# Kernel tuning notes

Hardware: AMD Instinct MI355X
Metric: run time of the kernel (lower is better)

The kernel has to match this reference:

```python
import jax, jax.numpy as jnp
import numpy as np

N = 100_000          # nodes
E = 1_600_000        # edges
NUM_LABELS = 1000
LBL_DIM = 64
BBOX_DIM = 64        # bbox MLP output dim
HID = 128            # gnn hidden = out channels; gnn in = LBL_DIM + BBOX_DIM = 128


def setup_inputs() -> dict:
    key = jax.random.key(0)
    ks = jax.random.split(key, 14)
    label = jax.random.randint(ks[0], (N,), 0, NUM_LABELS)
    bbox = jax.random.uniform(ks[1], (N, 4), dtype=jnp.float32)
    edge_index = jax.random.randint(ks[2], (2, E), 0, N)
    emb_table = jax.random.normal(ks[3], (NUM_LABELS, LBL_DIM), dtype=jnp.float32) * 0.02
    mlp_w1 = jax.random.normal(ks[4], (4, BBOX_DIM), dtype=jnp.float32) * 0.5
    mlp_b1 = jnp.zeros((BBOX_DIM,), jnp.float32)
    mlp_w2 = jax.random.normal(ks[5], (BBOX_DIM, BBOX_DIM), dtype=jnp.float32) * 0.125
    mlp_b2 = jnp.zeros((BBOX_DIM,), jnp.float32)
    w_g0 = jax.random.normal(ks[6], (HID, HID), dtype=jnp.float32) * 0.088
    b_g0 = jnp.zeros((HID,), jnp.float32)
    w_g1 = jax.random.normal(ks[7], (HID, HID), dtype=jnp.float32) * 0.088
    b_g1 = jnp.zeros((HID,), jnp.float32)
    w_g2 = jax.random.normal(ks[8], (HID, HID), dtype=jnp.float32) * 0.088
    b_g2 = jnp.zeros((HID,), jnp.float32)
    return dict(label=label, bbox=bbox, edge_index=edge_index, emb_table=emb_table,
                mlp_w1=mlp_w1, mlp_b1=mlp_b1, mlp_w2=mlp_w2, mlp_b2=mlp_b2,
                w_g0=w_g0, b_g0=b_g0, w_g1=w_g1, b_g1=b_g1, w_g2=w_g2, b_g2=b_g2)


def _gcn_norm(edge_index, n):
    # add self loops, compute symmetric normalization deg^-1/2 A_hat deg^-1/2
    loops = jnp.arange(n, dtype=edge_index.dtype)
    src = jnp.concatenate([edge_index[0], loops])
    dst = jnp.concatenate([edge_index[1], loops])
    deg = jax.ops.segment_sum(jnp.ones_like(dst, dtype=jnp.float32), dst, num_segments=n)
    dinv = jnp.where(deg > 0, jax.lax.rsqrt(deg), 0.0)
    norm = dinv[src] * dinv[dst]  # [E+N]
    return src, dst, norm


def _gcn_conv(x, src, dst, norm, w, b, n):
    h = x @ w                                   # [N, C]
    msg = h[src] * norm[:, None]                # gather + scale, [E+N, C]
    out = jax.ops.segment_sum(msg, dst, num_segments=n)  # scatter-add
    return out + b


def reference(label, bbox, edge_index, emb_table,
              mlp_w1, mlp_b1, mlp_w2, mlp_b2,
              w_g0, b_g0, w_g1, b_g1, w_g2, b_g2):
    n = bbox.shape[0]
    lbl = emb_table[label]                                  # [N, 64]
    h = jax.nn.relu(bbox @ mlp_w1 + mlp_b1) @ mlp_w2 + mlp_b2  # [N, 64]
    x = jnp.concatenate([lbl, h], axis=-1)                  # [N, 128]
    src, dst, norm = _gcn_norm(edge_index, n)
    x = jax.nn.relu(_gcn_conv(x, src, dst, norm, w_g0, b_g0, n))
    x = jax.nn.relu(_gcn_conv(x, src, dst, norm, w_g1, b_g1, n))
    x = _gcn_conv(x, src, dst, norm, w_g2, b_g2, n)
    return x
```

## Files before the change

kernel.cpp:

```cpp
#include <hip/hip_runtime.h>
#include <hip/hip_bf16.h>
#include <hip/hip_fp16.h>
#include <cstdint>
#include <cstddef>

typedef _Float16 h8 __attribute__((ext_vector_type(8)));
typedef float f4 __attribute__((ext_vector_type(4)));

#define CNT_PAD 16


__global__ __launch_bounds__(256) void k_count_rank(const int* __restrict__ dst, int* __restrict__ cnt_pad,
                                                    int* __restrict__ rank, int E) {
    int i = blockIdx.x * 256 + threadIdx.x;
    if (i < E) rank[i] = atomicAdd(&cnt_pad[(size_t)dst[i] * CNT_PAD], 1);
}

__global__ __launch_bounds__(256) void k_scan_a(const int* __restrict__ cnt_pad, int* __restrict__ offs,
                                                int* __restrict__ partials, float* __restrict__ dinv, int N) {
    __shared__ int sh[256];
    int t = threadIdx.x;
    int i = blockIdx.x * 256 + t;
    int v = (i < N) ? (cnt_pad[(size_t)i * CNT_PAD] + 1) : 0;
    sh[t] = v;
    __syncthreads();
    for (int d = 1; d < 256; d <<= 1) {
        int add = (t >= d) ? sh[t - d] : 0;
        __syncthreads();
        sh[t] += add;
        __syncthreads();
    }
    if (i < N) {
        offs[i] = sh[t] - v;
        dinv[i] = rsqrtf((float)v);
    }
    if (t == 255) partials[blockIdx.x] = sh[255];
}

__global__ __launch_bounds__(512) void k_scan_b(int* __restrict__ partials, int nb) {
    __shared__ int sh[512];
    int t = threadIdx.x;
    int v = (t < nb) ? partials[t] : 0;
    sh[t] = v;
    __syncthreads();
    for (int d = 1; d < 512; d <<= 1) {
        int add = (t >= d) ? sh[t - d] : 0;
        __syncthreads();
        sh[t] += add;
        __syncthreads();
    }
    if (t < nb) partials[t] = sh[t];
}

__global__ __launch_bounds__(256) void k_scan_c(int* __restrict__ offs, const int* __restrict__ partials,
                                                int N, int nb) {
    int i = blockIdx.x * 256 + threadIdx.x;
    if (i < N) {
        int b = i >> 8;
        if (b > 0) offs[i] += partials[b - 1];
    } else if (i == N) {
        offs[N] = partials[nb - 1];
    }
}

__global__ __launch_bounds__(256) void k_fill2(const int* __restrict__ src, const int* __restrict__ dst,
                                               const int* __restrict__ rank, const int* __restrict__ offs,
                                               const float* __restrict__ dinv,
                                               long long* __restrict__ cpack, int E) {
    int i = blockIdx.x * 256 + threadIdx.x;
    if (i < E) {
        int s = src[i], d = dst[i];
        int pos = offs[d] + rank[i];
        unsigned int nrm = (unsigned int)__float_as_int(dinv[s] * dinv[d]);
        long long v = ((long long)nrm << 32) | (unsigned int)s;
        __builtin_nontemporal_store(v, &cpack[pos]);
    }
}

__global__ __launch_bounds__(256) void k_fill_loops(const int* __restrict__ offs,
                                                    const float* __restrict__ dinv,
                                                    long long* __restrict__ cpack, int N) {
    int i = blockIdx.x * 256 + threadIdx.x;
    if (i < N) {
        float di = dinv[i];
        unsigned int nrm = (unsigned int)__float_as_int(di * di);
        long long v = ((long long)nrm << 32) | (unsigned int)i;
        __builtin_nontemporal_store(v, &cpack[offs[i + 1] - 1]);
    }
}


__global__ __launch_bounds__(256) void k_prep_w(const float* __restrict__ w0, const float* __restrict__ w1,
                                                const float* __restrict__ w2, _Float16* __restrict__ WT) {
    int idx = blockIdx.x * 256 + threadIdx.x;
    if (idx >= 3 * 16384) return;
    int l = idx >> 14, rem = idx & 16383, c = rem >> 7, k = rem & 127;
    const float* W = (l == 0) ? w0 : (l == 1) ? w1 : w2;
    WT[idx] = (_Float16)W[k * 128 + c];
}


__global__ __launch_bounds__(256) void k_feat(const int* __restrict__ label, const float* __restrict__ bbox,
                                              const float* __restrict__ emb,
                                              const float* __restrict__ w1, const float* __restrict__ b1,
                                              const float* __restrict__ w2, const float* __restrict__ b2,
                                              __half* __restrict__ X, int N) {
    __shared__ float w1s[4 * 64];
    __shared__ float b1s[64], b2s[64];
    __shared__ _Float16 w2t[64][72];
    __shared__ _Float16 h1s[32][72];

    int t = threadIdx.x;
    if (t < 256) w1s[t] = w1[t];
    if (t < 64) { b1s[t] = b1[t]; b2s[t] = b2[t]; }
    #pragma unroll
    for (int i = 0; i < 16; ++i) {
        int idx = t + i * 256;
        int k = idx >> 6, c = idx & 63;
        w2t[c][k] = (_Float16)w2[idx];
    }

    int wv = t >> 6, lane = t & 63;
    int r = lane & 15, q = lane >> 4;
    int blockBase = blockIdx.x * 32;
    int nb0 = __builtin_amdgcn_readfirstlane(blockBase + wv * 8);

    #pragma unroll
    for (int nn = 0; nn < 8; ++nn) {
        int node = nb0 + nn;
        float h1 = 0.f;
        if (node < N) {
            float bb0 = bbox[node * 4 + 0];
            float bb1 = bbox[node * 4 + 1];
            float bb2 = bbox[node * 4 + 2];
            float bb3 = bbox[node * 4 + 3];
            h1 = bb0 * w1s[lane] + bb1 * w1s[64 + lane]
               + bb2 * w1s[128 + lane] + bb3 * w1s[192 + lane] + b1s[lane];
            h1 = fmaxf(h1, 0.f);
            int lb = label[node];
            X[(size_t)node * 128 + lane] = __float2half(emb[(size_t)lb * 64 + lane]);
        }
        h1s[wv * 8 + nn][lane] = (_Float16)h1;
    }
    __syncthreads();

    int rt = wv & 1;
    int ch = wv >> 1;
    h8 a0 = *(const h8*)&h1s[rt * 16 + r][q * 8];
    h8 a1 = *(const h8*)&h1s[rt * 16 + r][32 + q * 8];
    #pragma unroll
    for (int ct = 0; ct < 2; ++ct) {
        int col = ch * 32 + ct * 16 + r;
        h8 bv0 = *(const h8*)&w2t[col][q * 8];
        h8 bv1 = *(const h8*)&w2t[col][32 + q * 8];
        f4 acc = {0.f, 0.f, 0.f, 0.f};
        acc = __builtin_amdgcn_mfma_f32_16x16x32_f16(a0, bv0, acc, 0, 0, 0);
        acc = __builtin_amdgcn_mfma_f32_16x16x32_f16(a1, bv1, acc, 0, 0, 0);
        float bb = b2s[col];
        #pragma unroll
        for (int i = 0; i < 4; ++i) {
            int node = blockBase + rt * 16 + q * 4 + i;
            if (node < N) X[(size_t)node * 128 + 64 + col] = __float2half(acc[i] + bb);
        }
    }
}


__global__ __launch_bounds__(256) void k_gemm_mfma(const _Float16* __restrict__ X,
                                                   const _Float16* __restrict__ WT,
                                                   _Float16* __restrict__ H, int N) {
    int t = threadIdx.x;
    int wv = t >> 6, lane = t & 63;
    int r = lane & 15, q = lane >> 4;
    int n0 = blockIdx.x * 64 + wv * 16;

    int arow = n0 + r; if (arow > N - 1) arow = N - 1;
    h8 a[4];
    #pragma unroll
    for (int s = 0; s < 4; ++s)
        a[s] = *(const h8*)&X[(size_t)arow * 128 + s * 32 + q * 8];

    #pragma unroll
    for (int ct = 0; ct < 8; ++ct) {
        h8 b[4];
        #pragma unroll
        for (int s = 0; s < 4; ++s)
            b[s] = *(const h8*)&WT[(size_t)(ct * 16 + r) * 128 + s * 32 + q * 8];
        f4 acc = {0.f, 0.f, 0.f, 0.f};
        #pragma unroll
        for (int s = 0; s < 4; ++s)
            acc = __builtin_amdgcn_mfma_f32_16x16x32_f16(a[s], b[s], acc, 0, 0, 0);
        #pragma unroll
        for (int i = 0; i < 4; ++i) {
            int row = n0 + q * 4 + i;
            if (row < N) H[(size_t)row * 128 + ct * 16 + r] = (_Float16)acc[i];
        }
    }
}


#define FMA8(hv, wv_)                                                                        \
    {                                                                                        \
        float2 f;                                                                            \
        f = __half22float2(*(const __half2*)&(hv).x); acc[0] += f.x * (wv_); acc[1] += f.y * (wv_); \
        f = __half22float2(*(const __half2*)&(hv).y); acc[2] += f.x * (wv_); acc[3] += f.y * (wv_); \
        f = __half22float2(*(const __half2*)&(hv).z); acc[4] += f.x * (wv_); acc[5] += f.y * (wv_); \
        f = __half22float2(*(const __half2*)&(hv).w); acc[6] += f.x * (wv_); acc[7] += f.y * (wv_); \
    }

template <int OUT_HALF>
__global__ __launch_bounds__(256) void k_agg(const uint4* __restrict__ H4, const int* __restrict__ offs,
                                             const int2* __restrict__ cpack,
                                             const float* __restrict__ bias, void* __restrict__ Yv,
                                             int N, int do_relu) {
    int node = blockIdx.x * 16 + (threadIdx.x >> 4);
    if (node >= N) return;
    int li = threadIdx.x & 15;
    int i0 = offs[node], i1 = offs[node + 1];

    float acc[8];
    #pragma unroll
    for (int k = 0; k < 8; ++k) acc[k] = 0.f;

    for (int base = i0; base < i1; base += 16) {
        int navail = i1 - base; if (navail > 16) navail = 16;
        int lidx = li < navail ? li : (navail - 1);
        int2 ep = cpack[base + lidx];

        float wA[4]; uint4 hA[4];
        #pragma unroll
        for (int j = 0; j < 4; ++j) {
            int cl = j < navail ? j : (navail - 1);
            int s = __shfl(ep.x, cl, 16);
            float wj = __int_as_float(__shfl(ep.y, cl, 16));
            wA[j] = j < navail ? wj : 0.f;
            hA[j] = H4[(size_t)s * 16 + li];
        }
        for (int e = 4; e < navail; e += 4) {
            float wB[4]; uint4 hB[4];
            #pragma unroll
            for (int j = 0; j < 4; ++j) {
                int idx = e + j;
                int cl = idx < navail ? idx : (navail - 1);
                int s = __shfl(ep.x, cl, 16);
                float wj = __int_as_float(__shfl(ep.y, cl, 16));
                wB[j] = idx < navail ? wj : 0.f;
                hB[j] = H4[(size_t)s * 16 + li];
            }
            #pragma unroll
            for (int j = 0; j < 4; ++j) FMA8(hA[j], wA[j]);
            #pragma unroll
            for (int j = 0; j < 4; ++j) { wA[j] = wB[j]; hA[j] = hB[j]; }
        }
        #pragma unroll
        for (int j = 0; j < 4; ++j) FMA8(hA[j], wA[j]);
    }

    float4 b0 = *(const float4*)&bias[li * 8];
    float4 b1 = *(const float4*)&bias[li * 8 + 4];
    acc[0] += b0.x; acc[1] += b0.y; acc[2] += b0.z; acc[3] += b0.w;
    acc[4] += b1.x; acc[5] += b1.y; acc[6] += b1.z; acc[7] += b1.w;
    if (do_relu) {
        #pragma unroll
        for (int k = 0; k < 8; ++k) acc[k] = fmaxf(acc[k], 0.f);
    }
    if (OUT_HALF) {
        __half2 p0 = __float22half2_rn(make_float2(acc[0], acc[1]));
        __half2 p1 = __float22half2_rn(make_float2(acc[2], acc[3]));
        __half2 p2 = __float22half2_rn(make_float2(acc[4], acc[5]));
        __half2 p3 = __float22half2_rn(make_float2(acc[6], acc[7]));
        uint4 pk;
        pk.x = *(unsigned int*)&p0; pk.y = *(unsigned int*)&p1;
        pk.z = *(unsigned int*)&p2; pk.w = *(unsigned int*)&p3;
        ((uint4*)Yv)[(size_t)node * 16 + li] = pk;
    } else {
        float* Yf = (float*)Yv;
        *(float4*)&Yf[(size_t)node * 128 + li * 8]     = make_float4(acc[0], acc[1], acc[2], acc[3]);
        *(float4*)&Yf[(size_t)node * 128 + li * 8 + 4] = make_float4(acc[4], acc[5], acc[6], acc[7]);
    }
}


extern "C" void kernel_launch(void* const* d_in, const int* in_sizes, int n_in,
                              void* d_out, int out_size, void* d_ws, size_t ws_size,
                              hipStream_t stream) {
    const int*   label = (const int*)d_in[0];
    const float* bbox  = (const float*)d_in[1];
    const int*   eidx  = (const int*)d_in[2];
    const float* emb   = (const float*)d_in[3];
    const float* w1    = (const float*)d_in[4];
    const float* b1    = (const float*)d_in[5];
    const float* w2    = (const float*)d_in[6];
    const float* b2    = (const float*)d_in[7];
    const float* wg0   = (const float*)d_in[8];
    const float* bg0   = (const float*)d_in[9];
    const float* wg1   = (const float*)d_in[10];
    const float* bg1   = (const float*)d_in[11];
    const float* wg2   = (const float*)d_in[12];
    const float* bg2   = (const float*)d_in[13];

    int N = in_sizes[0];
    int E = in_sizes[2] / 2;
    const int* esrc = eidx;
    const int* edst = eidx + E;

    char* ws = (char*)d_ws;
    int*       offs     = (int*)      (ws + 0x80000);
    int*       partials = (int*)      (ws + 0x100000);
    float*     dinv     = (float*)    (ws + 0x180000);
    _Float16*  WT       = (_Float16*) (ws + 0x1C0000);
    long long* cpack    = (long long*)(ws + 0x200000);
    __half*    F0       = (__half*)   (ws + 0x1000000);
    int*       cnt_pad  = (int*)      (ws + 0x1000000);
    int*       rank     = (int*)      (ws + 0x1800000);
    __half*    G        = (__half*)   (ws + 0x2900000);
    __half*    F1       = (__half*)   d_out;
    float*     Of       = (float*)    d_out;

    int nb = (N + 255) / 256;
    int eb = (E + 255) / 256;

    hipMemsetAsync(cnt_pad, 0, (size_t)N * CNT_PAD * 4, stream);
    k_count_rank<<<eb, 256, 0, stream>>>(edst, cnt_pad, rank, E);
    k_scan_a<<<nb, 256, 0, stream>>>(cnt_pad, offs, partials, dinv, N);
    k_scan_b<<<1, 512, 0, stream>>>(partials, nb);
    k_scan_c<<<(N + 1 + 255) / 256, 256, 0, stream>>>(offs, partials, N, nb);
    k_fill2<<<eb, 256, 0, stream>>>(esrc, edst, rank, offs, dinv, cpack, E);
    k_fill_loops<<<nb, 256, 0, stream>>>(offs, dinv, cpack, N);

    k_prep_w<<<192, 256, 0, stream>>>(wg0, wg1, wg2, WT);
    k_feat<<<(N + 31) / 32, 256, 0, stream>>>(label, bbox, emb, w1, b1, w2, b2, F0, N);

    int gemm_grid = (N + 63) / 64;
    int agg_grid  = (N + 15) / 16;

    k_gemm_mfma<<<gemm_grid, 256, 0, stream>>>((const _Float16*)F0, WT + 0 * 16384, (_Float16*)G, N);
    k_agg<1><<<agg_grid, 256, 0, stream>>>((const uint4*)G, offs, (const int2*)cpack, bg0, F1, N, 1);
    k_gemm_mfma<<<gemm_grid, 256, 0, stream>>>((const _Float16*)F1, WT + 1 * 16384, (_Float16*)G, N);
    k_agg<1><<<agg_grid, 256, 0, stream>>>((const uint4*)G, offs, (const int2*)cpack, bg1, F0, N, 1);
    k_gemm_mfma<<<gemm_grid, 256, 0, stream>>>((const _Float16*)F0, WT + 2 * 16384, (_Float16*)G, N);
    k_agg<0><<<agg_grid, 256, 0, stream>>>((const uint4*)G, offs, (const int2*)cpack, bg2, Of, N, 0);
}
```

Baseline: 438.9 us.

## Degree-sort aggregation nodes, fuse feature build with first GEMM, fold self-loop fill

Builds a degree histogram during the scan and scatters node ids into a permutation bucketed by in-degree. Each aggregation launch then walks nodes in that order, so 16-lane groups in a block handle nodes of similar degree and waste less time on load imbalance. The feature-construction kernel now keeps the 128-wide input row in shared memory and applies the first GCN weight GEMM directly, which drops one global write and read of the feature matrix and one kernel launch. Self-loop entry writes move into the scan-finalize kernel. The cost is extra atomics and a perm lookup per node, and the permutation breaks locality of output writes and offs reads.

```diff
diff --git a/kernel.cpp b/kernel.cpp
--- a/kernel.cpp
+++ b/kernel.cpp
@@ -17,13 +17,20 @@
 }
 
 __global__ __launch_bounds__(256) void k_scan_a(const int* __restrict__ cnt_pad, int* __restrict__ offs,
-                                                int* __restrict__ partials, float* __restrict__ dinv, int N) {
+                                                int* __restrict__ partials, float* __restrict__ dinv,
+                                                int* __restrict__ hist, int N) {
     __shared__ int sh[256];
+    __shared__ int lh[64];
     int t = threadIdx.x;
+    if (t < 64) lh[t] = 0;
     int i = blockIdx.x * 256 + t;
     int v = (i < N) ? (cnt_pad[(size_t)i * CNT_PAD] + 1) : 0;
     sh[t] = v;
     __syncthreads();
+    if (i < N) {
+        int b = v < 64 ? v : 63;
+        atomicAdd(&lh[b], 1);
+    }
     for (int d = 1; d < 256; d <<= 1) {
         int add = (t >= d) ? sh[t - d] : 0;
         __syncthreads();
@@ -35,13 +42,17 @@
         dinv[i] = rsqrtf((float)v);
     }
     if (t == 255) partials[blockIdx.x] = sh[255];
-}
-
-__global__ __launch_bounds__(512) void k_scan_b(int* __restrict__ partials, int nb) {
+    __syncthreads();
+    if (t < 64 && lh[t]) atomicAdd(&hist[t * CNT_PAD], lh[t]);
+}
+
+__global__ __launch_bounds__(512) void k_scan_b(int* __restrict__ partials, int* __restrict__ hist, int nb) {
     __shared__ int sh[512];
+    __shared__ int hs[64];
     int t = threadIdx.x;
     int v = (t < nb) ? partials[t] : 0;
     sh[t] = v;
+    if (t < 64) hs[t] = hist[t * CNT_PAD];
     __syncthreads();
     for (int d = 1; d < 512; d <<= 1) {
         int add = (t >= d) ? sh[t - d] : 0;
@@ -50,14 +61,28 @@
         __syncthreads();
     }
     if (t < nb) partials[t] = sh[t];
+    for (int d = 1; d < 64; d <<= 1) {
+        int add = (t >= d && t < 64) ? hs[t - d] : 0;
+        __syncthreads();
+        if (t < 64) hs[t] += add;
+        __syncthreads();
+    }
+    if (t < 64) hist[t * CNT_PAD] = t ? hs[t - 1] : 0;
 }
 
 __global__ __launch_bounds__(256) void k_scan_c(int* __restrict__ offs, const int* __restrict__ partials,
-                                                int N, int nb) {
+                                                const int* __restrict__ cnt_pad, const float* __restrict__ dinv,
+                                                long long* __restrict__ cpack, int N, int nb) {
     int i = blockIdx.x * 256 + threadIdx.x;
     if (i < N) {
         int b = i >> 8;
-        if (b > 0) offs[i] += partials[b - 1];
+        int o = offs[i] + (b > 0 ? partials[b - 1] : 0);
+        offs[i] = o;
+        int cnt = cnt_pad[(size_t)i * CNT_PAD];
+        float di = dinv[i];
+        unsigned int nrm = (unsigned int)__float_as_int(di * di);
+        long long v = ((long long)nrm << 32) | (unsigned int)i;
+        __builtin_nontemporal_store(v, &cpack[o + cnt]);
     } else if (i == N) {
         offs[N] = partials[nb - 1];
     }
@@ -77,15 +102,14 @@
     }
 }
 
-__global__ __launch_bounds__(256) void k_fill_loops(const int* __restrict__ offs,
-                                                    const float* __restrict__ dinv,
-                                                    long long* __restrict__ cpack, int N) {
+__global__ __launch_bounds__(256) void k_perm_scatter(const int* __restrict__ cnt_pad, int* __restrict__ hist,
+                                                      int* __restrict__ perm, int N) {
     int i = blockIdx.x * 256 + threadIdx.x;
     if (i < N) {
-        float di = dinv[i];
-        unsigned int nrm = (unsigned int)__float_as_int(di * di);
-        long long v = ((long long)nrm << 32) | (unsigned int)i;
-        __builtin_nontemporal_store(v, &cpack[offs[i + 1] - 1]);
+        int deg = cnt_pad[(size_t)i * CNT_PAD] + 1;
+        int b = deg < 64 ? deg : 63;
+        int pos = atomicAdd(&hist[b * CNT_PAD], 1);
+        perm[pos] = i;
     }
 }
 
@@ -100,15 +124,17 @@
 }
 
 
-__global__ __launch_bounds__(256) void k_feat(const int* __restrict__ label, const float* __restrict__ bbox,
-                                              const float* __restrict__ emb,
-                                              const float* __restrict__ w1, const float* __restrict__ b1,
-                                              const float* __restrict__ w2, const float* __restrict__ b2,
-                                              __half* __restrict__ X, int N) {
-    __shared__ float w1s[4 * 64];
+__global__ __launch_bounds__(256) void k_feat_gemm(const int* __restrict__ label, const float* __restrict__ bbox,
+                                                   const float* __restrict__ emb,
+                                                   const float* __restrict__ w1, const float* __restrict__ b1,
+                                                   const float* __restrict__ w2, const float* __restrict__ b2,
+                                                   const _Float16* __restrict__ WT0,
+                                                   _Float16* __restrict__ G0, int N) {
+    __shared__ float w1s[256];
     __shared__ float b1s[64], b2s[64];
     __shared__ _Float16 w2t[64][72];
     __shared__ _Float16 h1s[32][72];
+    __shared__ _Float16 Fl[32][136];
 
     int t = threadIdx.x;
     if (t < 256) w1s[t] = w1[t];
@@ -123,44 +149,65 @@
     int wv = t >> 6, lane = t & 63;
     int r = lane & 15, q = lane >> 4;
     int blockBase = blockIdx.x * 32;
-    int nb0 = __builtin_amdgcn_readfirstlane(blockBase + wv * 8);
+    int nb0 = blockBase + wv * 8;
 
     #pragma unroll
     for (int nn = 0; nn < 8; ++nn) {
         int node = nb0 + nn;
         float h1 = 0.f;
+        _Float16 ev = (_Float16)0.f;
         if (node < N) {
             float bb0 = bbox[node * 4 + 0];
             float bb1 = bbox[node * 4 + 1];
             float bb2 = bbox[node * 4 + 2];
             float bb3 = bbox[node * 4 + 3];
-            h1 = bb0 * w1s[lane] + bb1 * w1s[64 + lane]
-               + bb2 * w1s[128 + lane] + bb3 * w1s[192 + lane] + b1s[lane];
-            h1 = fmaxf(h1, 0.f);
-            int lb = label[node];
-            X[(size_t)node * 128 + lane] = __float2half(emb[(size_t)lb * 64 + lane]);
+            h1 = fmaxf(bb0 * w1s[lane] + bb1 * w1s[64 + lane]
+                     + bb2 * w1s[128 + lane] + bb3 * w1s[192 + lane] + b1s[lane], 0.f);
+            ev = (_Float16)emb[(size_t)label[node] * 64 + lane];
         }
         h1s[wv * 8 + nn][lane] = (_Float16)h1;
-    }
-    __syncthreads();
-
-    int rt = wv & 1;
-    int ch = wv >> 1;
-    h8 a0 = *(const h8*)&h1s[rt * 16 + r][q * 8];
-    h8 a1 = *(const h8*)&h1s[rt * 16 + r][32 + q * 8];
-    #pragma unroll
-    for (int ct = 0; ct < 2; ++ct) {
-        int col = ch * 32 + ct * 16 + r;
-        h8 bv0 = *(const h8*)&w2t[col][q * 8];
-        h8 bv1 = *(const h8*)&w2t[col][32 + q * 8];
-        f4 acc = {0.f, 0.f, 0.f, 0.f};
-        acc = __builtin_amdgcn_mfma_f32_16x16x32_f16(a0, bv0, acc, 0, 0, 0);
-        acc = __builtin_amdgcn_mfma_f32_16x16x32_f16(a1, bv1, acc, 0, 0, 0);
-        float bb = b2s[col];
-        #pragma unroll
-        for (int i = 0; i < 4; ++i) {
-            int node = blockBase + rt * 16 + q * 4 + i;
-            if (node < N) X[(size_t)node * 128 + 64 + col] = __float2half(acc[i] + bb);
+        Fl[wv * 8 + nn][lane] = ev;
+    }
+    __syncthreads();
+
+    int rt = wv & 1, ch = wv >> 1;
+    {
+        h8 a0 = *(const h8*)&h1s[rt * 16 + r][q * 8];
+        h8 a1 = *(const h8*)&h1s[rt * 16 + r][32 + q * 8];
+        #pragma unroll
+        for (int ct = 0; ct < 2; ++ct) {
+            int col = ch * 32 + ct * 16 + r;
+            h8 bv0 = *(const h8*)&w2t[col][q * 8];
+            h8 bv1 = *(const h8*)&w2t[col][32 + q * 8];
+            f4 acc = {0.f, 0.f, 0.f, 0.f};
+            acc = __builtin_amdgcn_mfma_f32_16x16x32_f16(a0, bv0, acc, 0, 0, 0);
+            acc = __builtin_amdgcn_mfma_f32_16x16x32_f16(a1, bv1, acc, 0, 0, 0);
+            float bb = b2s[col];
+            #pragma unroll
+            for (int i = 0; i < 4; ++i)
+                Fl[rt * 16 + q * 4 + i][64 + col] = (_Float16)(acc[i] + bb);
+        }
+    }
+    __syncthreads();
+
+    {
+        h8 a[4];
+        #pragma unroll
+        for (int s = 0; s < 4; ++s) a[s] = *(const h8*)&Fl[rt * 16 + r][s * 32 + q * 8];
+        #pragma unroll
+        for (int ct = 0; ct < 4; ++ct) {
+            int col = ch * 64 + ct * 16 + r;
+            f4 acc = {0.f, 0.f, 0.f, 0.f};
+            #pragma unroll
+            for (int s = 0; s < 4; ++s) {
+                h8 bv = *(const h8*)&WT0[(size_t)col * 128 + s * 32 + q * 8];
+                acc = __builtin_amdgcn_mfma_f32_16x16x32_f16(a[s], bv, acc, 0, 0, 0);
+            }
+            #pragma unroll
+            for (int i = 0; i < 4; ++i) {
+                int node = blockBase + rt * 16 + q * 4 + i;
+                if (node < N) G0[(size_t)node * 128 + col] = (_Float16)acc[i];
+            }
         }
     }
 }
@@ -210,11 +257,12 @@
 
 template <int OUT_HALF>
 __global__ __launch_bounds__(256) void k_agg(const uint4* __restrict__ H4, const int* __restrict__ offs,
-                                             const int2* __restrict__ cpack,
+                                             const int2* __restrict__ cpack, const int* __restrict__ perm,
                                              const float* __restrict__ bias, void* __restrict__ Yv,
                                              int N, int do_relu) {
-    int node = blockIdx.x * 16 + (threadIdx.x >> 4);
-    if (node >= N) return;
+    int slot = blockIdx.x * 16 + (threadIdx.x >> 4);
+    if (slot >= N) return;
+    int node = perm[slot];
     int li = threadIdx.x & 15;
     int i0 = offs[node], i1 = offs[node + 1];
 
@@ -305,39 +353,41 @@
     const int* edst = eidx + E;
 
     char* ws = (char*)d_ws;
-    int*       offs     = (int*)      (ws + 0x80000);
-    int*       partials = (int*)      (ws + 0x100000);
-    float*     dinv     = (float*)    (ws + 0x180000);
-    _Float16*  WT       = (_Float16*) (ws + 0x1C0000);
+    int*       offs     = (int*)      (ws + 0x000000);
+    float*     dinv     = (float*)    (ws + 0x070000);
+    int*       perm     = (int*)      (ws + 0x0E0000);
+    int*       partials = (int*)      (ws + 0x150000);
+    int*       hist     = (int*)      (ws + 0x158000);
+    _Float16*  WT       = (_Float16*) (ws + 0x160000);
     long long* cpack    = (long long*)(ws + 0x200000);
-    __half*    F0       = (__half*)   (ws + 0x1000000);
+    __half*    B        = (__half*)   (ws + 0x1000000);
     int*       cnt_pad  = (int*)      (ws + 0x1000000);
     int*       rank     = (int*)      (ws + 0x1800000);
-    __half*    G        = (__half*)   (ws + 0x2900000);
-    __half*    F1       = (__half*)   d_out;
+    __half*    A        = (__half*)   (ws + 0x2900000);
     float*     Of       = (float*)    d_out;
 
     int nb = (N + 255) / 256;
     int eb = (E + 255) / 256;
 
     hipMemsetAsync(cnt_pad, 0, (size_t)N * CNT_PAD * 4, stream);
+    hipMemsetAsync(hist, 0, 64 * CNT_PAD * 4, stream);
     k_count_rank<<<eb, 256, 0, stream>>>(edst, cnt_pad, rank, E);
-    k_scan_a<<<nb, 256, 0, stream>>>(cnt_pad, offs, partials, dinv, N);
-    k_scan_b<<<1, 512, 0, stream>>>(partials, nb);
-    k_scan_c<<<(N + 1 + 255) / 256, 256, 0, stream>>>(offs, partials, N, nb);
+    k_scan_a<<<nb, 256, 0, stream>>>(cnt_pad, offs, partials, dinv, hist, N);
+    k_scan_b<<<1, 512, 0, stream>>>(partials, hist, nb);
+    k_scan_c<<<(N + 1 + 255) / 256, 256, 0, stream>>>(offs, partials, cnt_pad, dinv, cpack, N, nb);
     k_fill2<<<eb, 256, 0, stream>>>(esrc, edst, rank, offs, dinv, cpack, E);
-    k_fill_loops<<<nb, 256, 0, stream>>>(offs, dinv, cpack, N);
+    k_perm_scatter<<<nb, 256, 0, stream>>>(cnt_pad, hist, perm, N);
 
     k_prep_w<<<192, 256, 0, stream>>>(wg0, wg1, wg2, WT);
-    k_feat<<<(N + 31) / 32, 256, 0, stream>>>(label, bbox, emb, w1, b1, w2, b2, F0, N);
+    k_feat_gemm<<<(N + 31) / 32, 256, 0, stream>>>(label, bbox, emb, w1, b1, w2, b2,
+                                                   WT + 0 * 16384, (_Float16*)A, N);
 
     int gemm_grid = (N + 63) / 64;
     int agg_grid  = (N + 15) / 16;
 
-    k_gemm_mfma<<<gemm_grid, 256, 0, stream>>>((const _Float16*)F0, WT + 0 * 16384, (_Float16*)G, N);
-    k_agg<1><<<agg_grid, 256, 0, stream>>>((const uint4*)G, offs, (const int2*)cpack, bg0, F1, N, 1);
-    k_gemm_mfma<<<gemm_grid, 256, 0, stream>>>((const _Float16*)F1, WT + 1 * 16384, (_Float16*)G, N);
-    k_agg<1><<<agg_grid, 256, 0, stream>>>((const uint4*)G, offs, (const int2*)cpack, bg1, F0, N, 1);
-    k_gemm_mfma<<<gemm_grid, 256, 0, stream>>>((const _Float16*)F0, WT + 2 * 16384, (_Float16*)G, N);
-    k_agg<0><<<agg_grid, 256, 0, stream>>>((const uint4*)G, offs, (const int2*)cpack, bg2, Of, N, 0);
-}
+    k_agg<1><<<agg_grid, 256, 0, stream>>>((const uint4*)A, offs, (const int2*)cpack, perm, bg0, B, N, 1);
+    k_gemm_mfma<<<gemm_grid, 256, 0, stream>>>((const _Float16*)B, WT + 1 * 16384, (_Float16*)A, N);
+    k_agg<1><<<agg_grid, 256, 0, stream>>>((const uint4*)A, offs, (const int2*)cpack, perm, bg1, B, N, 1);
+    k_gemm_mfma<<<gemm_grid, 256, 0, stream>>>((const _Float16*)B, WT + 2 * 16384, (_Float16*)A, N);
+    k_agg<0><<<agg_grid, 256, 0, stream>>>((const uint4*)A, offs, (const int2*)cpack, perm, bg2, Of, N, 0);
+}
```

After: 620.5 us. +41.4%, slower.
